# Kernel optimization log

Measured on AMD Instinct MI355X. Metric: run time of the kernel, lower is better.

## Reference

```python
import jax, jax.numpy as jnp
import numpy as np

NUM_EMB = 16384
EMB_DIM = 64
BETA = 0.25  # commitment_cost, legacy=True formulation


def _l2norm(x, axis=-1):
    # matches F.normalize(p=2): x / max(||x||, 1e-12)
    n = jnp.sqrt(jnp.sum(x * x, axis=axis, keepdims=True))
    return x / jnp.maximum(n, 1e-12)


def setup_inputs() -> dict:
    key = jax.random.key(0)
    k_z, k_cb, k_w, k_b = jax.random.split(key, 4)
    z = jax.random.normal(k_z, (16, 1024, EMB_DIM), dtype=jnp.float32)
    # frozen codebook: N(0, d^{-0.5})
    codebook = jax.random.normal(k_cb, (NUM_EMB, EMB_DIM), dtype=jnp.float32) * (EMB_DIM ** -0.5)
    # Linear(d, d) default init: U(-1/sqrt(d), 1/sqrt(d))
    lim = 1.0 / np.sqrt(EMB_DIM)
    proj_w = jax.random.uniform(k_w, (EMB_DIM, EMB_DIM), dtype=jnp.float32, minval=-lim, maxval=lim)
    proj_b = jax.random.uniform(k_b, (EMB_DIM,), dtype=jnp.float32, minval=-lim, maxval=lim)
    scale = jnp.float32(10.0)  # l2_norm_scale
    return {"z": z, "codebook": codebook, "proj_w": proj_w, "proj_b": proj_b, "scale": scale}


def reference(z, codebook, proj_w, proj_b, scale):
    B, T, d = z.shape
    zf = z.reshape(-1, d)                                   # [BT, d]
    quant_codebook = codebook @ proj_w.T + proj_b           # [N, d]
    zn = _l2norm(zf)
    cn = _l2norm(quant_codebook)
    distances = -jnp.einsum('bd,nd->bn', zn, cn) * scale    # [BT, N]
    idx = jnp.argmin(distances, axis=1)                     # [BT]
    quantized = quant_codebook[idx].reshape(z.shape)        # [B, T, d]
    sg = jax.lax.stop_gradient
    commitment_loss = jnp.mean((sg(quantized) - z) ** 2)
    codebook_loss = jnp.mean((quantized - sg(z)) ** 2)
    vq_loss = commitment_loss + BETA * codebook_loss        # legacy=True
    quantized_st = z + sg(quantized - z)                    # straight-through
    return quantized_st, vq_loss, idx.reshape(B, T)
```

## Files before the change

### kernel.cpp

```cpp
#include <hip/hip_runtime.h>
#include <hip/hip_bf16.h>


#define NCODES 16384
#define NTOK   16384
#define DIM    64
#define MARGIN_MFMA 8e-3f
#define CAP    16

typedef __attribute__((ext_vector_type(8))) short bf16x8;
typedef __attribute__((ext_vector_type(4))) float f32x4;
#define GLOBAL_AS __attribute__((address_space(1)))
#define LDS_AS    __attribute__((address_space(3)))

__device__ float  g_qcb[NCODES * DIM];
__device__ short  g_cnb[NCODES * DIM];
__device__ short  g_znb[NTOK * DIM];
__device__ unsigned g_topu[NTOK];
__device__ int    g_candcnt[NTOK];
__device__ int    g_cand[NTOK * CAP];
__device__ int    g_wl[NTOK];
__device__ int    g_wln;
__device__ float  g_partial[2048];

__device__ __forceinline__ float wave_sum64(float v) {
#pragma unroll
  for (int o = 32; o > 0; o >>= 1) v += __shfl_xor(v, o, 64);
  return v;
}
__device__ __forceinline__ short f2bf(float f) {
  __hip_bfloat16 h = __float2bfloat16(f);
  return *reinterpret_cast<short*>(&h);
}
__device__ __forceinline__ float bf2f(short s) {
  __hip_bfloat16 h = *reinterpret_cast<__hip_bfloat16*>(&s);
  return __bfloat162float(h);
}
__device__ __forceinline__ void split8(const float* v, bf16x8& hi, bf16x8& lo) {
#pragma unroll
  for (int i = 0; i < 8; ++i) {
    float f = v[i];
    short h = f2bf(f);
    hi[i] = h;
    lo[i] = f2bf(f - bf2f(h));
  }
}

__global__ __launch_bounds__(256) void k_prep(const float* __restrict__ cb,
                                              const float* __restrict__ pw,
                                              const float* __restrict__ pb,
                                              const float* __restrict__ z) {
  int tid = threadIdx.x;
  int wave = tid >> 6, lane = tid & 63, quad = lane >> 4, col = lane & 15;
  if (blockIdx.x < 1024) {
    __shared__ float pn[4][16];
    int rowBase = blockIdx.x * 16;
    const float* cr = cb + (size_t)(rowBase + col) * 64 + quad * 8;
    bf16x8 ah0, al0, ah1, al1;
    split8(cr, ah0, al0);
    split8(cr + 32, ah1, al1);
    const f32x4 fz = {0.f, 0.f, 0.f, 0.f};
    int j = wave * 16 + col;
    const float* wr = pw + (size_t)j * 64 + quad * 8;
    bf16x8 bh0, bl0, bh1, bl1;
    split8(wr, bh0, bl0);
    split8(wr + 32, bh1, bl1);
    f32x4 d = __builtin_amdgcn_mfma_f32_16x16x32_bf16(ah0, bh0, fz, 0, 0, 0);
    d = __builtin_amdgcn_mfma_f32_16x16x32_bf16(ah1, bh1, d, 0, 0, 0);
    d = __builtin_amdgcn_mfma_f32_16x16x32_bf16(ah0, bl0, d, 0, 0, 0);
    d = __builtin_amdgcn_mfma_f32_16x16x32_bf16(ah1, bl1, d, 0, 0, 0);
    d = __builtin_amdgcn_mfma_f32_16x16x32_bf16(al0, bh0, d, 0, 0, 0);
    d = __builtin_amdgcn_mfma_f32_16x16x32_bf16(al1, bh1, d, 0, 0, 0);
    float bj = pb[j];
    float vals[4], nr[4];
#pragma unroll
    for (int r = 0; r < 4; ++r) {
      float v = d[r] + bj;
      vals[r] = v;
      nr[r] = v * v;
    }
#pragma unroll
    for (int r = 0; r < 4; ++r) {
      float v = nr[r];
      v += __shfl_xor(v, 1, 64);
      v += __shfl_xor(v, 2, 64);
      v += __shfl_xor(v, 4, 64);
      v += __shfl_xor(v, 8, 64);
      nr[r] = v;
      if (col == 0) pn[wave][quad * 4 + r] = v;
    }
    __syncthreads();
#pragma unroll
    for (int r = 0; r < 4; ++r) {
      int row16 = quad * 4 + r;
      float tot = (pn[0][row16] + pn[1][row16]) + (pn[2][row16] + pn[3][row16]);
      float inv = 1.0f / fmaxf(sqrtf(tot), 1e-12f);
      int row = rowBase + row16;
      g_qcb[(size_t)row * 64 + j] = vals[r];
      g_cnb[(size_t)row * 64 + j] = f2bf(vals[r] * inv);
    }
  } else {
    int zb = blockIdx.x - 1024;
    int zgid = zb * 256 + tid;
    if (zgid < NTOK) { g_topu[zgid] = 0u; g_candcnt[zgid] = 0; }
    if (zgid == 0) g_wln = 0;
    int base = zb * 16;
    int row = base + wave * 4;
#pragma unroll
    for (int r = 0; r < 4; ++r) {
      float v = z[(size_t)(row + r) * 64 + lane];
      float tot = wave_sum64(v * v);
      g_znb[(size_t)(row + r) * 64 + lane] = f2bf(v / fmaxf(sqrtf(tot), 1e-12f));
    }
  }
}

__global__ __launch_bounds__(256) void k_mfma1() {
  __shared__ __align__(16) short smB[2][8192];
  int tid = threadIdx.x;
  int wave = tid >> 6, lane = tid & 63;
  int quad = lane >> 4, col = lane & 15;
  int tokGroup = blockIdx.x >> 4, split = blockIdx.x & 15;
  int tokBase = tokGroup * 256 + wave * 64;

  const short* za = g_znb + (size_t)(tokBase + col) * 64 + quad * 8;
  bf16x8 A0[4], A1[4];
#pragma unroll
  for (int f = 0; f < 4; ++f) {
    A0[f] = *(const bf16x8*)(za + f * 16 * 64);
    A1[f] = *(const bf16x8*)(za + f * 16 * 64 + 32);
  }
  float m[4][4];
#pragma unroll
  for (int f = 0; f < 4; ++f)
#pragma unroll
    for (int r = 0; r < 4; ++r) m[f][r] = -3.0e38f;

  const char* gsplit = (const char*)(g_cnb + (size_t)split * 1024 * 64);
  int x = col & 7;
  int s0off = ((quad ^ x) << 3);
  int s1off = (((4 | quad) ^ x) << 3);
  int goff[4];
#pragma unroll
  for (int i = 0; i < 4; ++i) {
    int cidx = wave * 256 + i * 64 + lane;
    int row = cidx >> 3, sw = cidx & 7;
    goff[i] = row * 128 + ((sw ^ (row & 7)) << 4);
  }

#pragma unroll
  for (int i = 0; i < 4; ++i)
    __builtin_amdgcn_global_load_lds((const GLOBAL_AS void*)(gsplit + goff[i]),
                                     (LDS_AS void*)(&smB[0][wave * 2048 + i * 512]), 16, 0, 0);
  __syncthreads();

  int p = 0;
  for (int s = 0; s < 8; ++s) {
    if (s < 7) {
      const char* gb = gsplit + (size_t)(s + 1) * 16384;
#pragma unroll
      for (int i = 0; i < 4; ++i)
        __builtin_amdgcn_global_load_lds((const GLOBAL_AS void*)(gb + goff[i]),
                                         (LDS_AS void*)(&smB[p ^ 1][wave * 2048 + i * 512]),
                                         16, 0, 0);
    }
    const short* bufp = smB[p];
#pragma unroll
    for (int h = 0; h < 2; ++h) {
      bf16x8 B0[4], B1[4];
#pragma unroll
      for (int t = 0; t < 4; ++t) {
        const short* lb = bufp + ((h * 4 + t) * 16 + col) * 64;
        B0[t] = *(const bf16x8*)(lb + s0off);
        B1[t] = *(const bf16x8*)(lb + s1off);
      }
#pragma unroll
      for (int t = 0; t < 4; ++t) {
#pragma unroll
        for (int f = 0; f < 4; ++f) {
          f32x4 acc = {0.f, 0.f, 0.f, 0.f};
          acc = __builtin_amdgcn_mfma_f32_16x16x32_bf16(A0[f], B0[t], acc, 0, 0, 0);
          acc = __builtin_amdgcn_mfma_f32_16x16x32_bf16(A1[f], B1[t], acc, 0, 0, 0);
#pragma unroll
          for (int r = 0; r < 4; ++r) m[f][r] = fmaxf(m[f][r], acc[r]);
        }
      }
    }
    __syncthreads();
    p ^= 1;
  }

#pragma unroll
  for (int f = 0; f < 4; ++f)
#pragma unroll
    for (int r = 0; r < 4; ++r) {
      float v = m[f][r];
      v = fmaxf(v, __shfl_xor(v, 1, 64));
      v = fmaxf(v, __shfl_xor(v, 2, 64));
      v = fmaxf(v, __shfl_xor(v, 4, 64));
      v = fmaxf(v, __shfl_xor(v, 8, 64));
      if (col == 0) {
        unsigned b = __float_as_uint(v);
        unsigned e = (b & 0x80000000u) ? ~b : (b | 0x80000000u);
        atomicMax(&g_topu[tokBase + f * 16 + quad * 4 + r], e);
      }
    }
}

__global__ __launch_bounds__(256) void k_mfma2() {
  __shared__ __align__(16) short smB[2][8192];
  int tid = threadIdx.x;
  int wave = tid >> 6, lane = tid & 63;
  int quad = lane >> 4, col = lane & 15;
  int tokGroup = blockIdx.x >> 4, split = blockIdx.x & 15;
  int tokBase = tokGroup * 256 + wave * 64;

  const short* za = g_znb + (size_t)(tokBase + col) * 64 + quad * 8;
  bf16x8 A0[4], A1[4];
#pragma unroll
  for (int f = 0; f < 4; ++f) {
    A0[f] = *(const bf16x8*)(za + f * 16 * 64);
    A1[f] = *(const bf16x8*)(za + f * 16 * 64 + 32);
  }
  float th[4][4];
#pragma unroll
  for (int f = 0; f < 4; ++f)
#pragma unroll
    for (int r = 0; r < 4; ++r) {
      unsigned u = g_topu[tokBase + f * 16 + quad * 4 + r];
      unsigned b = (u & 0x80000000u) ? (u & 0x7FFFFFFFu) : ~u;
      th[f][r] = __uint_as_float(b) - MARGIN_MFMA;
    }

  const char* gsplit = (const char*)(g_cnb + (size_t)split * 1024 * 64);
  int x = col & 7;
  int s0off = ((quad ^ x) << 3);
  int s1off = (((4 | quad) ^ x) << 3);
  int goff[4];
#pragma unroll
  for (int i = 0; i < 4; ++i) {
    int cidx = wave * 256 + i * 64 + lane;
    int row = cidx >> 3, sw = cidx & 7;
    goff[i] = row * 128 + ((sw ^ (row & 7)) << 4);
  }

#pragma unroll
  for (int i = 0; i < 4; ++i)
    __builtin_amdgcn_global_load_lds((const GLOBAL_AS void*)(gsplit + goff[i]),
                                     (LDS_AS void*)(&smB[0][wave * 2048 + i * 512]), 16, 0, 0);
  __syncthreads();

  int codeB = split * 1024 + col;
  int p = 0;
  for (int s = 0; s < 8; ++s) {
    if (s < 7) {
      const char* gb = gsplit + (size_t)(s + 1) * 16384;
#pragma unroll
      for (int i = 0; i < 4; ++i)
        __builtin_amdgcn_global_load_lds((const GLOBAL_AS void*)(gb + goff[i]),
                                         (LDS_AS void*)(&smB[p ^ 1][wave * 2048 + i * 512]),
                                         16, 0, 0);
    }
    const short* bufp = smB[p];
#pragma unroll
    for (int h = 0; h < 2; ++h) {
      bf16x8 B0[4], B1[4];
#pragma unroll
      for (int t = 0; t < 4; ++t) {
        const short* lb = bufp + ((h * 4 + t) * 16 + col) * 64;
        B0[t] = *(const bf16x8*)(lb + s0off);
        B1[t] = *(const bf16x8*)(lb + s1off);
      }
#pragma unroll
      for (int t = 0; t < 4; ++t) {
        int code = codeB + s * 128 + (h * 4 + t) * 16;
#pragma unroll
        for (int f = 0; f < 4; ++f) {
          f32x4 acc = {0.f, 0.f, 0.f, 0.f};
          acc = __builtin_amdgcn_mfma_f32_16x16x32_bf16(A0[f], B0[t], acc, 0, 0, 0);
          acc = __builtin_amdgcn_mfma_f32_16x16x32_bf16(A1[f], B1[t], acc, 0, 0, 0);
          float dmax = fmaxf(fmaxf(acc[0] - th[f][0], acc[1] - th[f][1]),
                             fmaxf(acc[2] - th[f][2], acc[3] - th[f][3]));
          if (dmax >= 0.f) {
#pragma unroll
            for (int r = 0; r < 4; ++r) {
              if (acc[r] >= th[f][r]) {
                int tok = tokBase + f * 16 + quad * 4 + r;
                int pos = atomicAdd(&g_candcnt[tok], 1);
                if (pos < CAP) g_cand[tok * CAP + pos] = code;
              }
            }
          }
        }
      }
    }
    __syncthreads();
    p ^= 1;
  }
}

__global__ __launch_bounds__(256) void k_scan() {
  __shared__ int flags[256];
  __shared__ int sbase;
  int tid = threadIdx.x;
  int tok = blockIdx.x * 256 + tid;
  int flag = (g_candcnt[tok] >= 2) ? 1 : 0;
  flags[tid] = flag;
  __syncthreads();
  if (tid == 0) {
    int run = 0;
    for (int i = 0; i < 256; ++i) {
      int f = flags[i];
      flags[i] = run;
      run += f;
    }
    sbase = atomicAdd(&g_wln, run);
  }
  __syncthreads();
  if (flag) g_wl[sbase + flags[tid]] = tok;
}

__global__ __launch_bounds__(256) void k_arb(const float* __restrict__ z,
                                             const float* __restrict__ cb,
                                             const float* __restrict__ pw,
                                             const float* __restrict__ pb) {
  __shared__ double WT[64 * 65];
  __shared__ float cbl[4][64];
  int tid = threadIdx.x;
  int wave = tid >> 6, lane = tid & 63;
  for (int e = tid; e < 4096; e += 256) {
    int j = e >> 6, k = e & 63;
    WT[k * 65 + j] = (double)pw[e];
  }
  __syncthreads();

  int wln = g_wln;
  double bj = (double)pb[lane];
  int gwave = blockIdx.x * 4 + wave;

  for (int e = gwave; e < wln; e += 4096) {
    int tok = g_wl[e];
    int cnt = g_candcnt[tok];
    double zj = (double)z[(size_t)tok * 64 + lane];
    double best = -1.0e300;
    int bi = 0x7FFFFFFF;
    int lim = (cnt <= CAP) ? cnt : 0;
    for (int c = 0; c < lim; ++c) {
      int code = g_cand[tok * CAP + c];
      cbl[wave][lane] = cb[(size_t)code * 64 + lane];
      double s0 = 0.0, s1 = 0.0, s2 = 0.0, s3 = 0.0;
#pragma unroll
      for (int kk = 0; kk < 16; ++kk) {
        s0 = fma(WT[kk * 65 + lane], (double)cbl[wave][kk], s0);
        s1 = fma(WT[(kk + 16) * 65 + lane], (double)cbl[wave][kk + 16], s1);
        s2 = fma(WT[(kk + 32) * 65 + lane], (double)cbl[wave][kk + 32], s2);
        s3 = fma(WT[(kk + 48) * 65 + lane], (double)cbl[wave][kk + 48], s3);
      }
      double qc = ((s0 + s1) + (s2 + s3)) + bj;
      double s = zj * qc, n2 = qc * qc;
#pragma unroll
      for (int o = 32; o > 0; o >>= 1) {
        s += __shfl_xor(s, o, 64);
        n2 += __shfl_xor(n2, o, 64);
      }
      double key = s / fmax(sqrt(n2), 1e-12);
      if (key > best || (key == best && code < bi)) { best = key; bi = code; }
    }
    if (cnt > CAP) {
      for (int code = 0; code < NCODES; ++code) {
        cbl[wave][lane] = cb[(size_t)code * 64 + lane];
        double s0 = 0.0, s1 = 0.0, s2 = 0.0, s3 = 0.0;
#pragma unroll
        for (int kk = 0; kk < 16; ++kk) {
          s0 = fma(WT[kk * 65 + lane], (double)cbl[wave][kk], s0);
          s1 = fma(WT[(kk + 16) * 65 + lane], (double)cbl[wave][kk + 16], s1);
          s2 = fma(WT[(kk + 32) * 65 + lane], (double)cbl[wave][kk + 32], s2);
          s3 = fma(WT[(kk + 48) * 65 + lane], (double)cbl[wave][kk + 48], s3);
        }
        double qc = ((s0 + s1) + (s2 + s3)) + bj;
        double s = zj * qc, n2 = qc * qc;
#pragma unroll
        for (int o = 32; o > 0; o >>= 1) {
          s += __shfl_xor(s, o, 64);
          n2 += __shfl_xor(n2, o, 64);
        }
        double key = s / fmax(sqrt(n2), 1e-12);
        if (key > best || (key == best && code < bi)) { best = key; bi = code; }
      }
    }
    if (lane == 0) g_cand[tok * CAP] = bi;
  }
}

__global__ __launch_bounds__(256) void k_out(const float* __restrict__ z,
                                             float* __restrict__ out0,
                                             float* __restrict__ out2) {
  __shared__ float ws[4];
  int tid = threadIdx.x;
  int wave = tid >> 6, lane = tid & 63;
  int base = blockIdx.x * 8 + wave * 2;
  int i0 = g_cand[(size_t)base * CAP];
  int i1 = g_cand[(size_t)(base + 1) * CAP];
  float q0 = g_qcb[(size_t)i0 * 64 + lane];
  float z0 = z[(size_t)base * 64 + lane];
  float q1 = g_qcb[(size_t)i1 * 64 + lane];
  float z1 = z[(size_t)(base + 1) * 64 + lane];
  float d0 = q0 - z0;
  float d1 = q1 - z1;
  out0[(size_t)base * 64 + lane] = z0 + d0;
  out0[(size_t)(base + 1) * 64 + lane] = z1 + d1;
  if (lane == 0) {
    out2[base] = (float)i0;
    out2[base + 1] = (float)i1;
  }
  float lsum = fmaf(d0, d0, d1 * d1);
  float tot = wave_sum64(lsum);
  if (lane == 0) ws[wave] = tot;
  __syncthreads();
  if (tid == 0) g_partial[blockIdx.x] = ((ws[0] + ws[1]) + (ws[2] + ws[3]));
}

__global__ void k_loss(float* __restrict__ out1) {
  int lane = threadIdx.x;
  float s = 0.f;
#pragma unroll
  for (int i = 0; i < 32; ++i) s += g_partial[lane + 64 * i];
  s = wave_sum64(s);
  if (lane == 0) out1[0] = 1.25f * s / 1048576.0f;
}

extern "C" void kernel_launch(void* const* d_in, const int* in_sizes, int n_in,
                              void* d_out, int out_size, void* d_ws, size_t ws_size,
                              hipStream_t stream) {
  const float* z = (const float*)d_in[0];
  const float* cb = (const float*)d_in[1];
  const float* pw = (const float*)d_in[2];
  const float* pb = (const float*)d_in[3];

  float* out0 = (float*)d_out;
  float* out1 = out0 + (size_t)NTOK * DIM;
  float* out2 = out1 + 1;

  hipLaunchKernelGGL(k_prep, dim3(2048), dim3(256), 0, stream, cb, pw, pb, z);
  hipLaunchKernelGGL(k_mfma1, dim3(1024), dim3(256), 0, stream);
  hipLaunchKernelGGL(k_mfma2, dim3(1024), dim3(256), 0, stream);
  hipLaunchKernelGGL(k_scan, dim3(64), dim3(256), 0, stream);
  hipLaunchKernelGGL(k_arb, dim3(1024), dim3(256), 0, stream, z, cb, pw, pb);
  hipLaunchKernelGGL(k_out, dim3(2048), dim3(256), 0, stream, z, out0, out2);
  hipLaunchKernelGGL(k_loss, dim3(1), dim3(64), 0, stream, out1);
}
```

Measured before the change: 190.7 us.

## Drop scan and loss kernels; fuse loss reduction via last-block atomic

Removes the k_scan worklist compaction: k_arb now walks its own fixed four tokens per wave and skips those with fewer than two candidates. Removes the separate k_loss launch: k_out publishes per-block partials with release atomics, and the last block to finish, found through an atomic counter, sums them. This cuts two kernel launches and their serial gaps. In exchange, k_arb work is spread unevenly across waves (no compaction), and a global atomic counter is added.

```diff
diff --git a/kernel.cpp b/kernel.cpp
--- a/kernel.cpp
+++ b/kernel.cpp
@@ -19,8 +19,7 @@
 __device__ unsigned g_topu[NTOK];
 __device__ int    g_candcnt[NTOK];
 __device__ int    g_cand[NTOK * CAP];
-__device__ int    g_wl[NTOK];
-__device__ int    g_wln;
+__device__ int    g_done;
 __device__ float  g_partial[2048];
 
 __device__ __forceinline__ float wave_sum64(float v) {
@@ -103,7 +102,7 @@
     int zb = blockIdx.x - 1024;
     int zgid = zb * 256 + tid;
     if (zgid < NTOK) { g_topu[zgid] = 0u; g_candcnt[zgid] = 0; }
-    if (zgid == 0) g_wln = 0;
+    if (zgid == 0) g_done = 0;
     int base = zb * 16;
     int row = base + wave * 4;
 #pragma unroll
@@ -297,27 +296,6 @@
     __syncthreads();
     p ^= 1;
   }
-}
-
-__global__ __launch_bounds__(256) void k_scan() {
-  __shared__ int flags[256];
-  __shared__ int sbase;
-  int tid = threadIdx.x;
-  int tok = blockIdx.x * 256 + tid;
-  int flag = (g_candcnt[tok] >= 2) ? 1 : 0;
-  flags[tid] = flag;
-  __syncthreads();
-  if (tid == 0) {
-    int run = 0;
-    for (int i = 0; i < 256; ++i) {
-      int f = flags[i];
-      flags[i] = run;
-      run += f;
-    }
-    sbase = atomicAdd(&g_wln, run);
-  }
-  __syncthreads();
-  if (flag) g_wl[sbase + flags[tid]] = tok;
 }
 
 __global__ __launch_bounds__(256) void k_arb(const float* __restrict__ z,
@@ -334,13 +312,13 @@
   }
   __syncthreads();
 
-  int wln = g_wln;
   double bj = (double)pb[lane];
   int gwave = blockIdx.x * 4 + wave;
 
-  for (int e = gwave; e < wln; e += 4096) {
-    int tok = g_wl[e];
+  for (int t4 = 0; t4 < 4; ++t4) {
+    int tok = gwave * 4 + t4;
     int cnt = g_candcnt[tok];
+    if (cnt < 2) continue;
     double zj = (double)z[(size_t)tok * 64 + lane];
     double best = -1.0e300;
     int bi = 0x7FFFFFFF;
@@ -394,8 +372,10 @@
 
 __global__ __launch_bounds__(256) void k_out(const float* __restrict__ z,
                                              float* __restrict__ out0,
+                                             float* __restrict__ out1,
                                              float* __restrict__ out2) {
   __shared__ float ws[4];
+  __shared__ int lastFlag;
   int tid = threadIdx.x;
   int wave = tid >> 6, lane = tid & 63;
   int base = blockIdx.x * 8 + wave * 2;
@@ -417,16 +397,24 @@
   float tot = wave_sum64(lsum);
   if (lane == 0) ws[wave] = tot;
   __syncthreads();
-  if (tid == 0) g_partial[blockIdx.x] = ((ws[0] + ws[1]) + (ws[2] + ws[3]));
-}
-
-__global__ void k_loss(float* __restrict__ out1) {
-  int lane = threadIdx.x;
-  float s = 0.f;
-#pragma unroll
-  for (int i = 0; i < 32; ++i) s += g_partial[lane + 64 * i];
-  s = wave_sum64(s);
-  if (lane == 0) out1[0] = 1.25f * s / 1048576.0f;
+  if (tid == 0) {
+    float p = ((ws[0] + ws[1]) + (ws[2] + ws[3]));
+    __hip_atomic_store(&g_partial[blockIdx.x], p, __ATOMIC_RELEASE,
+                       __HIP_MEMORY_SCOPE_AGENT);
+    int prev = __hip_atomic_fetch_add(&g_done, 1, __ATOMIC_ACQ_REL,
+                                      __HIP_MEMORY_SCOPE_AGENT);
+    lastFlag = (prev == 2047) ? 1 : 0;
+  }
+  __syncthreads();
+  if (lastFlag && wave == 0) {
+    float s = 0.f;
+#pragma unroll
+    for (int i = 0; i < 32; ++i)
+      s += __hip_atomic_load(&g_partial[lane + 64 * i], __ATOMIC_ACQUIRE,
+                             __HIP_MEMORY_SCOPE_AGENT);
+    s = wave_sum64(s);
+    if (lane == 0) out1[0] = 1.25f * s / 1048576.0f;
+  }
 }
 
 extern "C" void kernel_launch(void* const* d_in, const int* in_sizes, int n_in,
@@ -444,8 +432,6 @@
   hipLaunchKernelGGL(k_prep, dim3(2048), dim3(256), 0, stream, cb, pw, pb, z);
   hipLaunchKernelGGL(k_mfma1, dim3(1024), dim3(256), 0, stream);
   hipLaunchKernelGGL(k_mfma2, dim3(1024), dim3(256), 0, stream);
-  hipLaunchKernelGGL(k_scan, dim3(64), dim3(256), 0, stream);
   hipLaunchKernelGGL(k_arb, dim3(1024), dim3(256), 0, stream, z, cb, pw, pb);
-  hipLaunchKernelGGL(k_out, dim3(2048), dim3(256), 0, stream, z, out0, out2);
-  hipLaunchKernelGGL(k_loss, dim3(1), dim3(64), 0, stream, out1);
-}
+  hipLaunchKernelGGL(k_out, dim3(2048), dim3(256), 0, stream, z, out0, out1, out2);
+}
```

Result: slower. 279.2 us (+46.4%).
